# Optimization experiments

Hardware: AMD Instinct MI355X
Metric: run time of the kernel (lower is better)

## Reference

```python
import jax, jax.numpy as jnp
import numpy as np

N = 1024
DIM = 3
H = 64  # hidden width from sizes=[64, 64]


def _mlp(inp, W1, b1, W2, b2, W3, b3):
    # hk.nets.MLP(sizes + [1], activation=softplus): activate all but last layer
    h = jax.nn.softplus(inp @ W1 + b1)
    h = jax.nn.softplus(h @ W2 + b2)
    return h @ W3 + b3


def setup_inputs() -> dict:
    key = jax.random.key(0)
    ks = jax.random.split(key, 14)
    x = jax.random.normal(ks[0], (N, DIM), dtype=jnp.float32)
    t = jax.random.uniform(ks[1], (), dtype=jnp.float32)
    s = 0.01  # TruncatedNormal(0.01) init
    return {
        "x": x,
        "t": t,
        "xi_W1": jax.random.normal(ks[2], (2, H), jnp.float32) * s,
        "xi_b1": jnp.zeros((H,), jnp.float32),
        "xi_W2": jax.random.normal(ks[3], (H, H), jnp.float32) * s,
        "xi_b2": jnp.zeros((H,), jnp.float32),
        "xi_W3": jax.random.normal(ks[4], (H, 1), jnp.float32) * s,
        "xi_b3": jnp.zeros((1,), jnp.float32),
        "eta_W1": jax.random.normal(ks[5], (2, H), jnp.float32) * s,
        "eta_b1": jnp.zeros((H,), jnp.float32),
        "eta_W2": jax.random.normal(ks[6], (H, H), jnp.float32) * s,
        "eta_b2": jnp.zeros((H,), jnp.float32),
        "eta_W3": jax.random.normal(ks[7], (H, 1), jnp.float32) * s,
        "eta_b3": jnp.zeros((1,), jnp.float32),
    }


def reference(x, t, xi_W1, xi_b1, xi_W2, xi_b2, xi_W3, xi_b3,
              eta_W1, eta_b1, eta_W2, eta_b2, eta_W3, eta_b3):
    n = x.shape[0]
    # one-body term: xi(|x_i|, t) * x_i
    r = jnp.linalg.norm(x, axis=-1)  # (n,)
    inp_xi = jnp.stack([r, jnp.full_like(r, t)], axis=-1)  # (n, 2)
    res = _mlp(inp_xi, xi_W1, xi_b1, xi_W2, xi_b2, xi_W3, xi_b3) * x  # (n, dim)
    # two-body term: sum_j eta(|x_i - x_j|, t) * (x_i - x_j)
    rij = x[:, None, :] - x[None, :, :]  # (n, n, dim)
    eye = jnp.eye(n, dtype=x.dtype)
    rdist = jnp.linalg.norm(rij + eye[..., None], axis=-1) * (1.0 - eye)  # (n, n)
    inp_eta = jnp.stack([rdist, jnp.full_like(rdist, t)], axis=-1)  # (n, n, 2)
    eta_out = _mlp(inp_eta, eta_W1, eta_b1, eta_W2, eta_b2, eta_W3, eta_b3)  # (n, n, 1)
    res = res + (eta_out * rij).sum(axis=1)
    return res
```

## Files before the change

kernel.cpp:

```cpp
#include <hip/hip_runtime.h>
#include <math.h>


#define TABLE_N 512
#define RMAX 16.0f
#define NPART 1024
#define PBLK 33
#define XBLK 128
#define NFLAGS 264
#define DELTA (RMAX / (float)TABLE_N)
#define FLAG_OFF 1024
#define FLAG_MAGIC 0x9E3779B9u

__device__ __forceinline__ float sp_fast(float v) {
    return __logf(1.f + __expf(v));
}

__global__ __launch_bounds__(512, 1) void k_fused(
    const float* __restrict__ x, const float* __restrict__ t_ptr,
    const float* __restrict__ xiW1, const float* __restrict__ xib1,
    const float* __restrict__ xiW2, const float* __restrict__ xib2,
    const float* __restrict__ xiW3, const float* __restrict__ xib3,
    const float* __restrict__ eW1,  const float* __restrict__ eb1,
    const float* __restrict__ eW2,  const float* __restrict__ eb2,
    const float* __restrict__ eW3,  const float* __restrict__ eb3,
    float* __restrict__ ws, float* __restrict__ out)
{
    __shared__ __align__(16) float w2s[4096];
    __shared__ __align__(16) float w1s[128];
    __shared__ __align__(16) float b1s[64];
    __shared__ __align__(16) float b2s[64];
    __shared__ __align__(16) float w3s[64];
    __shared__ __align__(16) float hbuf[8][128];
    __shared__ __align__(16) float xsoa[3 * NPART];
    __shared__ __align__(16) float tab[516];

    const int tid = threadIdx.x;
    const int b   = blockIdx.x;
    const bool tb = (b < PBLK);

    const float* __restrict__ W1 = tb ? eW1 : xiW1;
    const float* __restrict__ B1 = tb ? eb1 : xib1;
    const float* __restrict__ W2 = tb ? eW2 : xiW2;
    const float* __restrict__ B2 = tb ? eb2 : xib2;
    const float* __restrict__ W3 = tb ? eW3 : xiW3;

    {
        const float4* src = (const float4*)W2;
        float4* dst = (float4*)w2s;
        dst[tid]       = src[tid];
        dst[tid + 512] = src[tid + 512];
        if (tid < 128)      w1s[tid]       = W1[tid];
        else if (tid < 192) b1s[tid - 128] = B1[tid - 128];
        else if (tid < 256) b2s[tid - 192] = B2[tid - 192];
        else if (tid < 320) w3s[tid - 256] = W3[tid - 256];
    }
    if (!tb) {
        const float4* src = (const float4*)x;
        float4* dst = (float4*)xsoa;
        dst[tid] = src[tid];
        if (tid < 256) dst[tid + 512] = src[tid + 512];
    }

    const float t  = t_ptr[0];
    const float B3 = tb ? eb3[0] : xib3[0];
    const int lane = tid & 63;
    const int w    = tid >> 6;
    __syncthreads();

    if (tb) {
        const int e0 = 16 * b + 2 * w;
        const int e1 = e0 + 1;
        const float r0 = (float)e0 * DELTA;
        const float r1 = (float)e1 * DELTA;
        const float w1a = w1s[lane], w1b = w1s[64 + lane], b1v = b1s[lane];
        hbuf[w][lane]      = sp_fast(fmaf(r0, w1a, fmaf(t, w1b, b1v)));
        hbuf[w][64 + lane] = sp_fast(fmaf(r1, w1a, fmaf(t, w1b, b1v)));
        float z0 = b2s[lane], z1 = z0;
        #pragma unroll
        for (int k = 0; k < 64; k += 4) {
            float4 ha = *(const float4*)&hbuf[w][k];
            float4 hb = *(const float4*)&hbuf[w][64 + k];
            float wa  = w2s[k * 64 + lane];
            float wbv = w2s[(k + 1) * 64 + lane];
            float wc  = w2s[(k + 2) * 64 + lane];
            float wd  = w2s[(k + 3) * 64 + lane];
            z0 = fmaf(ha.x, wa,  z0); z1 = fmaf(hb.x, wa,  z1);
            z0 = fmaf(ha.y, wbv, z0); z1 = fmaf(hb.y, wbv, z1);
            z0 = fmaf(ha.z, wc,  z0); z1 = fmaf(hb.z, wc,  z1);
            z0 = fmaf(ha.w, wd,  z0); z1 = fmaf(hb.w, wd,  z1);
        }
        float q0 = sp_fast(z0) * w3s[lane];
        float q1 = sp_fast(z1) * w3s[lane];
        #pragma unroll
        for (int off = 32; off > 0; off >>= 1) {
            q0 += __shfl_xor(q0, off);
            q1 += __shfl_xor(q1, off);
        }
        if (lane == 0) {
            if (e0 <= TABLE_N)
                __hip_atomic_store(&ws[e0], q0 + B3, __ATOMIC_RELAXED,
                                   __HIP_MEMORY_SCOPE_AGENT);
            if (e1 <= TABLE_N)
                __hip_atomic_store(&ws[e1], q1 + B3, __ATOMIC_RELAXED,
                                   __HIP_MEMORY_SCOPE_AGENT);
            asm volatile("s_waitcnt vmcnt(0)" ::: "memory");
            __hip_atomic_store((unsigned int*)ws + FLAG_OFF + 8 * b + w,
                               FLAG_MAGIC, __ATOMIC_RELAXED,
                               __HIP_MEMORY_SCOPE_AGENT);
        }
        return;
    }

    const int i = 8 * (b - PBLK) + w;
    const float xi0 = xsoa[3 * i], yi0 = xsoa[3 * i + 1], zi0 = xsoa[3 * i + 2];
    const float r0 = sqrtf(fmaf(xi0, xi0, fmaf(yi0, yi0, zi0 * zi0)));

    const float w1a = w1s[lane], w1b = w1s[64 + lane], b1v = b1s[lane];
    hbuf[w][lane] = sp_fast(fmaf(r0, w1a, fmaf(t, w1b, b1v)));
    float z0 = b2s[lane];
    #pragma unroll
    for (int k = 0; k < 64; k += 4) {
        float4 ha = *(const float4*)&hbuf[w][k];
        z0 = fmaf(ha.x, w2s[k * 64 + lane],       z0);
        z0 = fmaf(ha.y, w2s[(k + 1) * 64 + lane], z0);
        z0 = fmaf(ha.z, w2s[(k + 2) * 64 + lane], z0);
        z0 = fmaf(ha.w, w2s[(k + 3) * 64 + lane], z0);
    }
    float q0 = sp_fast(z0) * w3s[lane];
    #pragma unroll
    for (int off = 32; off > 0; off >>= 1) q0 += __shfl_xor(q0, off);
    const float fxi = q0 + B3;

    if (tid < NFLAGS) {
        const unsigned int* fl = (const unsigned int*)ws + FLAG_OFF + tid;
        unsigned int v = __hip_atomic_load(fl, __ATOMIC_RELAXED,
                                           __HIP_MEMORY_SCOPE_AGENT);
        int it = 0;
        while (v != FLAG_MAGIC) {
            __builtin_amdgcn_s_sleep(1);
            v = ((++it & 31) == 0)
                  ? __hip_atomic_load(fl, __ATOMIC_ACQUIRE,
                                      __HIP_MEMORY_SCOPE_AGENT)
                  : __hip_atomic_load(fl, __ATOMIC_RELAXED,
                                      __HIP_MEMORY_SCOPE_AGENT);
        }
    }
    __syncthreads();
    {
        tab[tid] = __hip_atomic_load(&ws[tid], __ATOMIC_RELAXED,
                                     __HIP_MEMORY_SCOPE_AGENT);
        if (tid == 0)
            tab[512] = __hip_atomic_load(&ws[512], __ATOMIC_RELAXED,
                                         __HIP_MEMORY_SCOPE_AGENT);
    }
    __syncthreads();

    float ax = 0.f, ay = 0.f, az = 0.f;
    const float scale = (float)TABLE_N / RMAX;
    #pragma unroll
    for (int it = 0; it < NPART / 64; ++it) {
        int j = it * 64 + lane;
        float dx = xi0 - xsoa[3 * j];
        float dy = yi0 - xsoa[3 * j + 1];
        float dz = zi0 - xsoa[3 * j + 2];
        float r = sqrtf(fmaf(dx, dx, fmaf(dy, dy, dz * dz)));
        float u = fminf(r * scale, (float)TABLE_N - 0.001f);
        int i0 = (int)u;
        float fr = u - (float)i0;
        float t0 = tab[i0], t1v = tab[i0 + 1];
        float f = fmaf(fr, t1v - t0, t0);
        ax = fmaf(f, dx, ax);
        ay = fmaf(f, dy, ay);
        az = fmaf(f, dz, az);
    }
    #pragma unroll
    for (int off = 32; off > 0; off >>= 1) {
        ax += __shfl_xor(ax, off);
        ay += __shfl_xor(ay, off);
        az += __shfl_xor(az, off);
    }
    if (lane == 0) {
        out[3 * i]     = fmaf(fxi, xi0, ax);
        out[3 * i + 1] = fmaf(fxi, yi0, ay);
        out[3 * i + 2] = fmaf(fxi, zi0, az);
    }
}

extern "C" void kernel_launch(void* const* d_in, const int* in_sizes, int n_in,
                              void* d_out, int out_size, void* d_ws, size_t ws_size,
                              hipStream_t stream) {
    const float* x     = (const float*)d_in[0];
    const float* t     = (const float*)d_in[1];
    const float* xiW1  = (const float*)d_in[2];
    const float* xib1  = (const float*)d_in[3];
    const float* xiW2  = (const float*)d_in[4];
    const float* xib2  = (const float*)d_in[5];
    const float* xiW3  = (const float*)d_in[6];
    const float* xib3  = (const float*)d_in[7];
    const float* eW1   = (const float*)d_in[8];
    const float* eb1   = (const float*)d_in[9];
    const float* eW2   = (const float*)d_in[10];
    const float* eb2   = (const float*)d_in[11];
    const float* eW3   = (const float*)d_in[12];
    const float* eb3   = (const float*)d_in[13];
    float* out = (float*)d_out;
    float* ws  = (float*)d_ws;

    k_fused<<<PBLK + XBLK, 512, 0, stream>>>(
        x, t, xiW1, xib1, xiW2, xib2, xiW3, xib3,
        eW1, eb1, eW2, eb2, eW3, eb3, ws, out);
}
```

Baseline: 85.15 us.

## Spread eta table build over more blocks; use float4 positions and paired table

Table-building blocks now compute one table entry per wavefront instead of two, which doubles the producer blocks and the flags consumers must wait on. Particle positions are staged in shared memory as padded float4 for single vector loads. The interpolation table is repacked as float2 pairs so each lookup is one LDS read. The repack costs an extra barrier, and the extra producer blocks add grid-level work and more flag polling.

```diff
diff --git a/kernel.cpp b/kernel.cpp
--- a/kernel.cpp
+++ b/kernel.cpp
@@ -5,9 +5,9 @@
 #define TABLE_N 512
 #define RMAX 16.0f
 #define NPART 1024
-#define PBLK 33
+#define PBLK 65
 #define XBLK 128
-#define NFLAGS 264
+#define NFLAGS 520
 #define DELTA (RMAX / (float)TABLE_N)
 #define FLAG_OFF 1024
 #define FLAG_MAGIC 0x9E3779B9u
@@ -31,9 +31,10 @@
     __shared__ __align__(16) float b1s[64];
     __shared__ __align__(16) float b2s[64];
     __shared__ __align__(16) float w3s[64];
-    __shared__ __align__(16) float hbuf[8][128];
-    __shared__ __align__(16) float xsoa[3 * NPART];
+    __shared__ __align__(16) float hbuf[8][64];
+    __shared__ __align__(16) float4 x4[NPART];
     __shared__ __align__(16) float tab[516];
+    __shared__ __align__(16) float2 tab2[513];
 
     const int tid = threadIdx.x;
     const int b   = blockIdx.x;
@@ -56,10 +57,11 @@
         else if (tid < 320) w3s[tid - 256] = W3[tid - 256];
     }
     if (!tb) {
-        const float4* src = (const float4*)x;
-        float4* dst = (float4*)xsoa;
-        dst[tid] = src[tid];
-        if (tid < 256) dst[tid + 512] = src[tid + 512];
+        #pragma unroll
+        for (int j = tid; j < NPART; j += 512) {
+            float a = x[3 * j], c = x[3 * j + 1], d = x[3 * j + 2];
+            x4[j] = make_float4(a, c, d, 0.f);
+        }
     }
 
     const float t  = t_ptr[0];
@@ -69,40 +71,24 @@
     __syncthreads();
 
     if (tb) {
-        const int e0 = 16 * b + 2 * w;
-        const int e1 = e0 + 1;
-        const float r0 = (float)e0 * DELTA;
-        const float r1 = (float)e1 * DELTA;
-        const float w1a = w1s[lane], w1b = w1s[64 + lane], b1v = b1s[lane];
-        hbuf[w][lane]      = sp_fast(fmaf(r0, w1a, fmaf(t, w1b, b1v)));
-        hbuf[w][64 + lane] = sp_fast(fmaf(r1, w1a, fmaf(t, w1b, b1v)));
-        float z0 = b2s[lane], z1 = z0;
+        const int e = 8 * b + w;
+        const float r0 = (float)e * DELTA;
+        hbuf[w][lane] = sp_fast(fmaf(r0, w1s[lane], fmaf(t, w1s[64 + lane], b1s[lane])));
+        float z0 = b2s[lane];
         #pragma unroll
         for (int k = 0; k < 64; k += 4) {
             float4 ha = *(const float4*)&hbuf[w][k];
-            float4 hb = *(const float4*)&hbuf[w][64 + k];
-            float wa  = w2s[k * 64 + lane];
-            float wbv = w2s[(k + 1) * 64 + lane];
-            float wc  = w2s[(k + 2) * 64 + lane];
-            float wd  = w2s[(k + 3) * 64 + lane];
-            z0 = fmaf(ha.x, wa,  z0); z1 = fmaf(hb.x, wa,  z1);
-            z0 = fmaf(ha.y, wbv, z0); z1 = fmaf(hb.y, wbv, z1);
-            z0 = fmaf(ha.z, wc,  z0); z1 = fmaf(hb.z, wc,  z1);
-            z0 = fmaf(ha.w, wd,  z0); z1 = fmaf(hb.w, wd,  z1);
+            z0 = fmaf(ha.x, w2s[k * 64 + lane],       z0);
+            z0 = fmaf(ha.y, w2s[(k + 1) * 64 + lane], z0);
+            z0 = fmaf(ha.z, w2s[(k + 2) * 64 + lane], z0);
+            z0 = fmaf(ha.w, w2s[(k + 3) * 64 + lane], z0);
         }
         float q0 = sp_fast(z0) * w3s[lane];
-        float q1 = sp_fast(z1) * w3s[lane];
         #pragma unroll
-        for (int off = 32; off > 0; off >>= 1) {
-            q0 += __shfl_xor(q0, off);
-            q1 += __shfl_xor(q1, off);
-        }
+        for (int off = 32; off > 0; off >>= 1) q0 += __shfl_xor(q0, off);
         if (lane == 0) {
-            if (e0 <= TABLE_N)
-                __hip_atomic_store(&ws[e0], q0 + B3, __ATOMIC_RELAXED,
-                                   __HIP_MEMORY_SCOPE_AGENT);
-            if (e1 <= TABLE_N)
-                __hip_atomic_store(&ws[e1], q1 + B3, __ATOMIC_RELAXED,
+            if (e <= TABLE_N)
+                __hip_atomic_store(&ws[e], q0 + B3, __ATOMIC_RELAXED,
                                    __HIP_MEMORY_SCOPE_AGENT);
             asm volatile("s_waitcnt vmcnt(0)" ::: "memory");
             __hip_atomic_store((unsigned int*)ws + FLAG_OFF + 8 * b + w,
@@ -113,11 +99,11 @@
     }
 
     const int i = 8 * (b - PBLK) + w;
-    const float xi0 = xsoa[3 * i], yi0 = xsoa[3 * i + 1], zi0 = xsoa[3 * i + 2];
+    const float4 pi = x4[i];
+    const float xi0 = pi.x, yi0 = pi.y, zi0 = pi.z;
     const float r0 = sqrtf(fmaf(xi0, xi0, fmaf(yi0, yi0, zi0 * zi0)));
 
-    const float w1a = w1s[lane], w1b = w1s[64 + lane], b1v = b1s[lane];
-    hbuf[w][lane] = sp_fast(fmaf(r0, w1a, fmaf(t, w1b, b1v)));
+    hbuf[w][lane] = sp_fast(fmaf(r0, w1s[lane], fmaf(t, w1s[64 + lane], b1s[lane])));
     float z0 = b2s[lane];
     #pragma unroll
     for (int k = 0; k < 64; k += 4) {
@@ -132,8 +118,8 @@
     for (int off = 32; off > 0; off >>= 1) q0 += __shfl_xor(q0, off);
     const float fxi = q0 + B3;
 
-    if (tid < NFLAGS) {
-        const unsigned int* fl = (const unsigned int*)ws + FLAG_OFF + tid;
+    for (int f = tid; f < NFLAGS; f += 512) {
+        const unsigned int* fl = (const unsigned int*)ws + FLAG_OFF + f;
         unsigned int v = __hip_atomic_load(fl, __ATOMIC_RELAXED,
                                            __HIP_MEMORY_SCOPE_AGENT);
         int it = 0;
@@ -155,21 +141,22 @@
                                          __HIP_MEMORY_SCOPE_AGENT);
     }
     __syncthreads();
+    if (tid < 512) tab2[tid] = make_float2(tab[tid], tab[tid + 1]);
+    __syncthreads();
 
     float ax = 0.f, ay = 0.f, az = 0.f;
     const float scale = (float)TABLE_N / RMAX;
     #pragma unroll
     for (int it = 0; it < NPART / 64; ++it) {
         int j = it * 64 + lane;
-        float dx = xi0 - xsoa[3 * j];
-        float dy = yi0 - xsoa[3 * j + 1];
-        float dz = zi0 - xsoa[3 * j + 2];
+        float4 pj = x4[j];
+        float dx = xi0 - pj.x, dy = yi0 - pj.y, dz = zi0 - pj.z;
         float r = sqrtf(fmaf(dx, dx, fmaf(dy, dy, dz * dz)));
         float u = fminf(r * scale, (float)TABLE_N - 0.001f);
         int i0 = (int)u;
         float fr = u - (float)i0;
-        float t0 = tab[i0], t1v = tab[i0 + 1];
-        float f = fmaf(fr, t1v - t0, t0);
+        float2 tt = tab2[i0];
+        float f = fmaf(fr, tt.y - tt.x, tt.x);
         ax = fmaf(f, dx, ax);
         ay = fmaf(f, dy, ay);
         az = fmaf(f, dz, az);
```

After: 85.78 us (median of 2 runs). About the same (+0.7%).
